# Performance work log

Measured on AMD Instinct MI355X. Metric: run time of the kernel, lower is better.

Reference implementation:

```python
import jax, jax.numpy as jnp
import numpy as np

HEADS = 8
DIM_HEAD = 64
DIM = 512
HIDDEN = HEADS * DIM_HEAD  # 512


def setup_inputs() -> dict:
    key = jax.random.key(0)
    k1, k2, k3, k4 = jax.random.split(key, 4)
    b, m, n = 4, 8, 512
    x = jax.random.normal(k1, (b, m, n, DIM), dtype=jnp.float32)
    pos_bias = jax.random.normal(k2, (HEADS, n, 16, 16), dtype=jnp.float32)
    # torch nn.Linear(dim, 3*hidden) weight is [3*hidden, dim]; we store the
    # transposed matmul form [dim, 3*hidden] for y = x @ W.
    w_qkv = jax.random.normal(k3, (DIM, 3 * HIDDEN), dtype=jnp.float32) * (DIM ** -0.5)
    w_out = jax.random.normal(k4, (HIDDEN, DIM), dtype=jnp.float32) * (HIDDEN ** -0.5)
    return {"x": x, "pos_bias": pos_bias, "w_qkv": w_qkv, "w_out": w_out}


def reference(x, pos_bias, w_qkv, w_out):
    b, m, n, _ = x.shape
    h, d = HEADS, DIM_HEAD
    scale = d ** -0.5
    qkv = jnp.einsum('bmnc,ce->bmne', x, w_qkv)  # [b,m,n,3*hidden]
    q, k, v = jnp.split(qkv, 3, axis=-1)
    # 'b m n (h d) -> (b m) h n d'
    def to_heads(t):
        return t.reshape(b * m, n, h, d).transpose(0, 2, 1, 3)
    q, k, v = to_heads(q), to_heads(k), to_heads(v)
    q = q * scale
    sim = jnp.einsum('bhid,bhjd->bhij', q, k)  # [(b*m), h, n, n]
    # pos_bias [h, n, p, q] -> mean over last two dims -> [h, n] -> broadcast [1,h,n,1]
    pb = pos_bias.mean(axis=(-2, -1))[None, :, :, None]
    sim = sim + pb
    sim = sim - jax.lax.stop_gradient(jnp.max(sim, axis=-1, keepdims=True))
    attn = jax.nn.softmax(sim, axis=-1)
    out = jnp.einsum('bhij,bhjd->bhid', attn, v)  # [(b*m), h, n, d]
    # '(b m) h n d -> b m n (h d)'
    out = out.transpose(0, 2, 1, 3).reshape(b, m, n, h * d)
    return jnp.einsum('bmne,ec->bmnc', out, w_out)
```

## Files before the change

### kernel.cpp

```cpp
#include <hip/hip_runtime.h>
#include <stdint.h>


typedef __attribute__((ext_vector_type(8))) short bf16x8;
typedef __attribute__((ext_vector_type(4))) float f32x4;
typedef __attribute__((ext_vector_type(4))) unsigned short us4;
typedef __attribute__((ext_vector_type(4))) float float4v;

__device__ __forceinline__ unsigned short f2b(float f) {
  union { float f; uint32_t u; } x; x.f = f;
  uint32_t r = x.u + 0x7fffu + ((x.u >> 16) & 1u);
  return (unsigned short)(r >> 16);
}

__device__ __forceinline__ uint32_t cvtpk(float lo, float hi) {
  uint32_t r;
  asm("v_cvt_pk_bf16_f32 %0, %1, %2" : "=v"(r) : "v"(lo), "v"(hi));
  return r;
}

__device__ __forceinline__ f32x4 mfma16(bf16x8 a, bf16x8 b, f32x4 c) {
  return __builtin_amdgcn_mfma_f32_16x16x32_bf16(a, b, c, 0, 0, 0);
}

__device__ __forceinline__ void gload_lds16(const unsigned short* g, unsigned short* l) {
  __builtin_amdgcn_global_load_lds(
      (const __attribute__((address_space(1))) unsigned int*)g,
      (__attribute__((address_space(3))) unsigned int*)l, 16, 0, 0);
}

__global__ __launch_bounds__(256) void cast_x_kernel(
    const float* __restrict__ src, unsigned short* __restrict__ dst) {
  size_t i = ((size_t)blockIdx.x * 256 + threadIdx.x) * 4;
  float4v v = *(const float4v*)(src + i);
  us4 o;
#pragma unroll
  for (int j = 0; j < 4; ++j) o[j] = f2b(v[j]);
  *(us4*)(dst + i) = o;
}

__global__ __launch_bounds__(256) void transpose_cast_kernel(
    const float* __restrict__ src, unsigned short* __restrict__ dst, int R, int C) {
  __shared__ float tile[64][65];
  const int tc0 = blockIdx.x * 64;
  const int tr0 = blockIdx.y * 64;
#pragma unroll
  for (int k2 = 0; k2 < 16; ++k2) {
    int idx = threadIdx.x + k2 * 256;
    int r = idx >> 6, c = idx & 63;
    tile[r][c] = src[(size_t)(tr0 + r) * C + tc0 + c];
  }
  __syncthreads();
#pragma unroll
  for (int k2 = 0; k2 < 16; ++k2) {
    int idx = threadIdx.x + k2 * 256;
    int c = idx >> 6, r = idx & 63;
    dst[(size_t)(tc0 + c) * R + tr0 + r] = f2b(tile[r][c]);
  }
}

__device__ __forceinline__ void gemm_core(
    const unsigned short* __restrict__ A, const unsigned short* __restrict__ Bt,
    int K, int r0, int c0, unsigned short* As, unsigned short* Bs,
    f32x4 (&acc)[4][4]) {
  const int tid = threadIdx.x;
  const int lane = tid & 63;
  const int wave = tid >> 6;
  const int wr = (wave >> 1) * 64;
  const int wc = (wave & 1) * 64;
  const int l15 = lane & 15;
  const int g = lane >> 4;
  const int lsw = l15 & 7;

#pragma unroll
  for (int m = 0; m < 4; ++m)
#pragma unroll
    for (int n = 0; n < 4; ++n) acc[m][n] = (f32x4){0.f, 0.f, 0.f, 0.f};

  for (int kt = 0; kt < K; kt += 64) {
#pragma unroll
    for (int i = 0; i < 4; ++i) {
      int chunk = tid + i * 256;
      int row = chunk >> 3;
      int csw = (chunk & 7) ^ (row & 7);
      gload_lds16(A + (size_t)(r0 + row) * K + kt + csw * 8, As + chunk * 8);
      gload_lds16(Bt + (size_t)(c0 + row) * K + kt + csw * 8, Bs + chunk * 8);
    }
    __syncthreads();
#pragma unroll
    for (int ks = 0; ks < 2; ++ks) {
      bf16x8 af[4], bfr[4];
      const int j = g + ks * 4;
      const int cj = (j ^ lsw) * 8;
#pragma unroll
      for (int m = 0; m < 4; ++m)
        af[m] = *(const bf16x8*)(As + (wr + m * 16 + l15) * 64 + cj);
#pragma unroll
      for (int n = 0; n < 4; ++n)
        bfr[n] = *(const bf16x8*)(Bs + (wc + n * 16 + l15) * 64 + cj);
#pragma unroll
      for (int m = 0; m < 4; ++m)
#pragma unroll
        for (int n = 0; n < 4; ++n) acc[m][n] = mfma16(af[m], bfr[n], acc[m][n]);
    }
    __syncthreads();
  }
}

__global__ __launch_bounds__(256) void gemm_qkv_kernel(
    const unsigned short* __restrict__ xb, const unsigned short* __restrict__ wqbT,
    unsigned short* __restrict__ qb, unsigned short* __restrict__ kb,
    unsigned short* __restrict__ vtb) {
  __shared__ unsigned short smem[16384];
  f32x4 acc[4][4];
  const int r0 = blockIdx.x * 128;
  const int c0 = blockIdx.y * 128;
  gemm_core(xb, wqbT, 512, r0, c0, smem, smem + 8192, acc);

  const int tid = threadIdx.x, lane = tid & 63, wave = tid >> 6;
  const int wr = (wave >> 1) * 64, wc = (wave & 1) * 64;
  const int l15 = lane & 15, g = lane >> 4;
  const int part = c0 >> 9;
  const float scl = (part == 0) ? 0.125f : 1.0f;

  if (part < 2) {
#pragma unroll
    for (int m = 0; m < 4; ++m) {
      int rbase = wr + m * 16 + 4 * g;
#pragma unroll
      for (int n = 0; n < 4; ++n) {
        int c = wc + n * 16 + l15;
        int c2 = c >> 3, ci = c & 7;
#pragma unroll
        for (int rr = 0; rr < 4; ++rr) {
          int r = rbase + rr;
          smem[r * 128 + ((c2 ^ (r & 15)) << 3) + ci] = f2b(acc[m][n][rr] * scl);
        }
      }
    }
    __syncthreads();
    unsigned short* dstb = (part == 0) ? qb : kb;
#pragma unroll
    for (int it = 0; it < 8; ++it) {
      int idx = tid + it * 256;
      int r = idx >> 4, c2 = idx & 15;
      bf16x8 v = *(const bf16x8*)(smem + r * 128 + ((c2 ^ (r & 15)) << 3));
      int e = c0 + c2 * 8;
      int rem = e & 511, h = rem >> 6, d = rem & 63;
      int ig = r0 + r;
      int bh = (ig >> 9) * 8 + h, i = ig & 511;
      *(bf16x8*)(dstb + ((size_t)bh * 512 + i) * 64 + d) = v;
    }
  } else {
#pragma unroll
    for (int m = 0; m < 4; ++m) {
      int rbase = wr + m * 16 + 4 * g;
      int r2 = rbase >> 3, rhalf = rbase & 7;
#pragma unroll
      for (int n = 0; n < 4; ++n) {
        int c = wc + n * 16 + l15;
        us4 v;
#pragma unroll
        for (int rr = 0; rr < 4; ++rr) v[rr] = f2b(acc[m][n][rr]);
        *(us4*)(smem + c * 128 + ((r2 ^ (c & 15)) << 3) + rhalf) = v;
      }
    }
    __syncthreads();
#pragma unroll
    for (int it = 0; it < 8; ++it) {
      int idx = tid + it * 256;
      int c = idx >> 4, r8 = idx & 15;
      bf16x8 v = *(const bf16x8*)(smem + c * 128 + ((r8 ^ (c & 15)) << 3));
      int e = c0 + c;
      int rem = e & 511, h = rem >> 6, d = rem & 63;
      int ig0 = r0 + r8 * 8;
      int bh = (ig0 >> 9) * 8 + h, i = ig0 & 511;
      *(bf16x8*)(vtb + ((size_t)bh * 64 + d) * 512 + i) = v;
    }
  }
}

__global__ __launch_bounds__(256) void gemm_out_kernel(
    const unsigned short* __restrict__ ao, const unsigned short* __restrict__ wobT,
    float* __restrict__ out) {
  __shared__ unsigned short smem[16384];
  f32x4 acc[4][4];
  const int r0 = blockIdx.x * 128;
  const int c0 = blockIdx.y * 128;
  gemm_core(ao, wobT, 512, r0, c0, smem, smem + 8192, acc);

  const int tid = threadIdx.x, lane = tid & 63, wave = tid >> 6;
  const int wr = (wave >> 1) * 64, wc = (wave & 1) * 64;
  const int l15 = lane & 15, g = lane >> 4;
#pragma unroll
  for (int m = 0; m < 4; ++m) {
    int i0g = r0 + wr + m * 16 + 4 * g;
#pragma unroll
    for (int n = 0; n < 4; ++n) {
      int e = c0 + wc + n * 16 + l15;
#pragma unroll
      for (int rr = 0; rr < 4; ++rr)
        out[(size_t)(i0g + rr) * 512 + e] = acc[m][n][rr];
    }
  }
}

__global__ __launch_bounds__(512, 4) void attn_kernel(
    const unsigned short* __restrict__ qb, const unsigned short* __restrict__ kb,
    const unsigned short* __restrict__ vtb, unsigned short* __restrict__ ao) {
  __shared__ unsigned short kbuf[2][8192];
  __shared__ unsigned short vbuf[2][8192];
  __shared__ unsigned short Ps[8][16][40];
  const int bh = blockIdx.x;
  const int qt = blockIdx.y;
  const int tid = threadIdx.x, lane = tid & 63, wave = tid >> 6;
  const int l15 = lane & 15, g = lane >> 4;
  const int qrow0 = qt * 128 + wave * 16;

  const unsigned short* Q = qb + ((size_t)bh * 512 + qrow0) * 64;
  const unsigned short* Kp = kb + (size_t)bh * 512 * 64;
  const unsigned short* Vt = vtb + (size_t)bh * 64 * 512;

  bf16x8 qf0 = *(const bf16x8*)(Q + l15 * 64 + g * 8);
  bf16x8 qf1 = *(const bf16x8*)(Q + l15 * 64 + 32 + g * 8);

  const int krow = tid >> 3;
  const int kck = (tid & 7) ^ (krow & 7);
  const int vrow = tid >> 4;
  const int vck = (tid & 15) ^ (vrow & 15);

  auto stage = [&](int t, int b) {
    const unsigned short* ks = Kp + ((size_t)t * 128 + krow) * 64 + kck * 8;
    gload_lds16(ks, kbuf[b] + tid * 8);
    gload_lds16(ks + 64 * 64, kbuf[b] + tid * 8 + 4096);
    const unsigned short* vs = Vt + (size_t)vrow * 512 + t * 128 + vck * 8;
    gload_lds16(vs, vbuf[b] + tid * 8);
    gload_lds16(vs + 32 * 512, vbuf[b] + tid * 8 + 4096);
  };

  f32x4 oacc[4];
#pragma unroll
  for (int m = 0; m < 4; ++m) oacc[m] = (f32x4){0.f, 0.f, 0.f, 0.f};
  float srow[4] = {0.f, 0.f, 0.f, 0.f};

  stage(0, 0);
  asm volatile("s_waitcnt vmcnt(0)" ::: "memory");
  __builtin_amdgcn_s_barrier();

  int cur = 0;
#pragma unroll
  for (int t = 0; t < 4; ++t) {
    if (t < 3) stage(t + 1, cur ^ 1);

    const unsigned short* kb_ = kbuf[cur];
    f32x4 s[8];
    const int c0i = g ^ (l15 & 7);
    __builtin_amdgcn_s_setprio(1);
#pragma unroll
    for (int tt = 0; tt < 8; ++tt) {
      int row = tt * 16 + l15;
      bf16x8 b0 = *(const bf16x8*)(kb_ + (row * 8 + c0i) * 8);
      bf16x8 b1 = *(const bf16x8*)(kb_ + (row * 8 + (c0i ^ 4)) * 8);
      f32x4 c = (f32x4){0.f, 0.f, 0.f, 0.f};
      c = mfma16(qf0, b0, c);
      s[tt] = mfma16(qf1, b1, c);
    }
    __builtin_amdgcn_s_setprio(0);

#pragma unroll
    for (int tt = 0; tt < 8; ++tt)
#pragma unroll
      for (int rr = 0; rr < 4; ++rr) {
        float e = __expf(s[tt][rr]);
        s[tt][rr] = e;
        srow[rr] += e;
      }

    const unsigned short* vb_ = vbuf[cur];
#pragma unroll
    for (int cc = 0; cc < 4; ++cc) {
#pragma unroll
      for (int rr = 0; rr < 4; ++rr) {
        uint32_t pk = cvtpk(s[cc * 2][rr], s[cc * 2 + 1][rr]);
        Ps[wave][4 * g + rr][l15] = (unsigned short)pk;
        Ps[wave][4 * g + rr][16 + l15] = (unsigned short)(pk >> 16);
      }
      asm volatile("s_waitcnt lgkmcnt(0)" ::: "memory");
      bf16x8 pf = *(const bf16x8*)(&Ps[wave][l15][g * 8]);
      __builtin_amdgcn_s_setprio(1);
#pragma unroll
      for (int m = 0; m < 4; ++m) {
        int vr = m * 16 + l15;
        bf16x8 vf = *(const bf16x8*)(vb_ + (vr * 16 + ((cc * 4 + g) ^ l15)) * 8);
        oacc[m] = mfma16(vf, pf, oacc[m]);
      }
      __builtin_amdgcn_s_setprio(0);
    }

    if (t < 3) {
      asm volatile("s_waitcnt vmcnt(0)" ::: "memory");
      __builtin_amdgcn_s_barrier();
      cur ^= 1;
    }
  }

#pragma unroll
  for (int rr = 0; rr < 4; ++rr)
#pragma unroll
    for (int o = 1; o < 16; o <<= 1) srow[rr] += __shfl_xor(srow[rr], o);
  int srcl = (l15 >> 2) * 16;
  float t0 = __shfl(srow[0], srcl), t1 = __shfl(srow[1], srcl);
  float t2 = __shfl(srow[2], srcl), t3 = __shfl(srow[3], srcl);
  int rq = l15 & 3;
  float sq = rq == 0 ? t0 : rq == 1 ? t1 : rq == 2 ? t2 : t3;
  float invq = 1.0f / sq;

  const int hh = bh & 7, bm = bh >> 3;
  unsigned short* aorow = ao + ((size_t)bm * 512 + qrow0 + l15) * 512 + hh * 64;
#pragma unroll
  for (int m = 0; m < 4; ++m) {
    union { us4 u; uint32_t w[2]; } uv;
    uv.w[0] = cvtpk(oacc[m][0] * invq, oacc[m][1] * invq);
    uv.w[1] = cvtpk(oacc[m][2] * invq, oacc[m][3] * invq);
    *(us4*)(aorow + m * 16 + 4 * g) = uv.u;
  }
}

extern "C" void kernel_launch(void* const* d_in, const int* in_sizes, int n_in,
                              void* d_out, int out_size, void* d_ws, size_t ws_size,
                              hipStream_t stream) {
  const float* x = (const float*)d_in[0];
  const float* w_qkv = (const float*)d_in[2];
  const float* w_out = (const float*)d_in[3];
  float* out = (float*)d_out;

  char* ws = (char*)d_ws;
  const size_t SZ_XB = 16384ull * 512 * 2;
  const size_t SZ_WQ = 1536ull * 512 * 2;
  const size_t SZ_WO = 512ull * 512 * 2;
  const size_t SZ_HB = 256ull * 512 * 64 * 2;
  unsigned short* xb = (unsigned short*)(ws);
  unsigned short* wqbT = (unsigned short*)(ws + SZ_XB);
  unsigned short* wobT = (unsigned short*)(ws + SZ_XB + SZ_WQ);
  unsigned short* qb = (unsigned short*)(ws + SZ_XB + SZ_WQ + SZ_WO);
  unsigned short* kb = (unsigned short*)(ws + SZ_XB + SZ_WQ + SZ_WO + SZ_HB);
  unsigned short* vtb = (unsigned short*)(ws + SZ_XB + SZ_WQ + SZ_WO + 2 * SZ_HB);
  unsigned short* ao = (unsigned short*)(ws + SZ_XB + SZ_WQ + SZ_WO + 3 * SZ_HB);

  cast_x_kernel<<<8192, 256, 0, stream>>>(x, xb);
  transpose_cast_kernel<<<dim3(1536 / 64, 512 / 64), 256, 0, stream>>>(w_qkv, wqbT, 512, 1536);
  transpose_cast_kernel<<<dim3(512 / 64, 512 / 64), 256, 0, stream>>>(w_out, wobT, 512, 512);
  gemm_qkv_kernel<<<dim3(128, 12), 256, 0, stream>>>(xb, wqbT, qb, kb, vtb);
  attn_kernel<<<dim3(256, 4), 512, 0, stream>>>(qb, kb, vtb, ao);
  gemm_out_kernel<<<dim3(128, 4), 256, 0, stream>>>(ao, wobT, out);
}
```

Before: 104.0 us.

## Fuse prep kernels, pipeline GEMM K-loop, shrink attention KV tiles

Merges the x cast and both weight transpose-casts into one launch, and folds the q scale into the transposed weight. The GEMM core becomes a 4-stage, 32-wide K pipeline with partial vmcnt waits, so loads overlap MFMAs. The attention kernel now uses 64-key tiles over 8 iterations with half-size LDS buffers and raised launch bounds to fit more blocks per CU. This trades more barriers and iterations for less launch overhead, better latency hiding and higher occupancy.

```diff
diff --git a/kernel.cpp b/kernel.cpp
--- a/kernel.cpp
+++ b/kernel.cpp
@@ -29,21 +29,34 @@
       (__attribute__((address_space(3))) unsigned int*)l, 16, 0, 0);
 }
 
-__global__ __launch_bounds__(256) void cast_x_kernel(
-    const float* __restrict__ src, unsigned short* __restrict__ dst) {
-  size_t i = ((size_t)blockIdx.x * 256 + threadIdx.x) * 4;
-  float4v v = *(const float4v*)(src + i);
-  us4 o;
-#pragma unroll
-  for (int j = 0; j < 4; ++j) o[j] = f2b(v[j]);
-  *(us4*)(dst + i) = o;
-}
-
-__global__ __launch_bounds__(256) void transpose_cast_kernel(
-    const float* __restrict__ src, unsigned short* __restrict__ dst, int R, int C) {
+__global__ __launch_bounds__(256) void prep_kernel(
+    const float* __restrict__ x, unsigned short* __restrict__ xb,
+    const float* __restrict__ wq, unsigned short* __restrict__ wqbT,
+    const float* __restrict__ wo, unsigned short* __restrict__ wobT) {
+  const int bid = blockIdx.x;
+  if (bid < 8192) {
+    size_t i = ((size_t)bid * 256 + threadIdx.x) * 4;
+    float4v v = *(const float4v*)(x + i);
+    us4 o;
+#pragma unroll
+    for (int j = 0; j < 4; ++j) o[j] = f2b(v[j]);
+    *(us4*)(xb + i) = o;
+    return;
+  }
   __shared__ float tile[64][65];
-  const int tc0 = blockIdx.x * 64;
-  const int tr0 = blockIdx.y * 64;
+  const float* src;
+  unsigned short* dst;
+  int R, C, bx, by;
+  float scl = 1.0f;
+  if (bid < 8192 + 192) {
+    int q = bid - 8192;
+    src = wq; dst = wqbT; R = 512; C = 1536; bx = q % 24; by = q / 24;
+    if (bx * 64 < 512) scl = 0.125f;
+  } else {
+    int q = bid - 8384;
+    src = wo; dst = wobT; R = 512; C = 512; bx = q % 8; by = q / 8;
+  }
+  const int tc0 = bx * 64, tr0 = by * 64;
 #pragma unroll
   for (int k2 = 0; k2 < 16; ++k2) {
     int idx = threadIdx.x + k2 * 256;
@@ -55,13 +68,13 @@
   for (int k2 = 0; k2 < 16; ++k2) {
     int idx = threadIdx.x + k2 * 256;
     int c = idx >> 6, r = idx & 63;
-    dst[(size_t)(tc0 + c) * R + tr0 + r] = f2b(tile[r][c]);
+    dst[(size_t)(tc0 + c) * R + tr0 + r] = f2b(tile[r][c] * scl);
   }
 }
 
 __device__ __forceinline__ void gemm_core(
     const unsigned short* __restrict__ A, const unsigned short* __restrict__ Bt,
-    int K, int r0, int c0, unsigned short* As, unsigned short* Bs,
+    int r0, int c0, unsigned short* As, unsigned short* Bs,
     f32x4 (&acc)[4][4]) {
   const int tid = threadIdx.x;
   const int lane = tid & 63;
@@ -70,58 +83,72 @@
   const int wc = (wave & 1) * 64;
   const int l15 = lane & 15;
   const int g = lane >> 4;
-  const int lsw = l15 & 7;
+  const int rsw = (l15 >> 1) & 3;
 
 #pragma unroll
   for (int m = 0; m < 4; ++m)
 #pragma unroll
     for (int n = 0; n < 4; ++n) acc[m][n] = (f32x4){0.f, 0.f, 0.f, 0.f};
 
-  for (int kt = 0; kt < K; kt += 64) {
-#pragma unroll
-    for (int i = 0; i < 4; ++i) {
+  auto stage_half = [&](int t) {
+    const int off = ((t >> 1) & 1) * 8192 + (t & 1) * 4096;
+    const int kt = t * 32;
+#pragma unroll
+    for (int i = 0; i < 2; ++i) {
       int chunk = tid + i * 256;
-      int row = chunk >> 3;
-      int csw = (chunk & 7) ^ (row & 7);
-      gload_lds16(A + (size_t)(r0 + row) * K + kt + csw * 8, As + chunk * 8);
-      gload_lds16(Bt + (size_t)(c0 + row) * K + kt + csw * 8, Bs + chunk * 8);
-    }
-    __syncthreads();
-#pragma unroll
-    for (int ks = 0; ks < 2; ++ks) {
-      bf16x8 af[4], bfr[4];
-      const int j = g + ks * 4;
-      const int cj = (j ^ lsw) * 8;
-#pragma unroll
-      for (int m = 0; m < 4; ++m)
-        af[m] = *(const bf16x8*)(As + (wr + m * 16 + l15) * 64 + cj);
-#pragma unroll
-      for (int n = 0; n < 4; ++n)
-        bfr[n] = *(const bf16x8*)(Bs + (wc + n * 16 + l15) * 64 + cj);
-#pragma unroll
-      for (int m = 0; m < 4; ++m)
-#pragma unroll
-        for (int n = 0; n < 4; ++n) acc[m][n] = mfma16(af[m], bfr[n], acc[m][n]);
-    }
-    __syncthreads();
-  }
+      int row = chunk >> 2;
+      int cg = (chunk & 3) ^ ((row >> 1) & 3);
+      gload_lds16(A + (size_t)(r0 + row) * 512 + kt + cg * 8, As + off + chunk * 8);
+      gload_lds16(Bt + (size_t)(c0 + row) * 512 + kt + cg * 8, Bs + off + chunk * 8);
+    }
+  };
+
+  stage_half(0);
+  stage_half(1);
+  stage_half(2);
+
+#pragma unroll
+  for (int t = 0; t < 16; ++t) {
+    if (t <= 13)      asm volatile("s_waitcnt vmcnt(8)" ::: "memory");
+    else if (t == 14) asm volatile("s_waitcnt vmcnt(4)" ::: "memory");
+    else              asm volatile("s_waitcnt vmcnt(0)" ::: "memory");
+    __builtin_amdgcn_s_barrier();
+    if (t + 3 < 16) stage_half(t + 3);
+    const int off = ((t >> 1) & 1) * 8192 + (t & 1) * 4096;
+    const unsigned short* as = As + off;
+    const unsigned short* bs = Bs + off;
+    bf16x8 af[4], bfr[4];
+#pragma unroll
+    for (int m = 0; m < 4; ++m)
+      af[m] = *(const bf16x8*)(as + ((wr + m * 16 + l15) * 4 + (g ^ rsw)) * 8);
+#pragma unroll
+    for (int n = 0; n < 4; ++n)
+      bfr[n] = *(const bf16x8*)(bs + ((wc + n * 16 + l15) * 4 + (g ^ rsw)) * 8);
+    __builtin_amdgcn_s_setprio(1);
+#pragma unroll
+    for (int m = 0; m < 4; ++m)
+#pragma unroll
+      for (int n = 0; n < 4; ++n) acc[m][n] = mfma16(af[m], bfr[n], acc[m][n]);
+    __builtin_amdgcn_s_setprio(0);
+  }
+  __syncthreads();
 }
 
 __global__ __launch_bounds__(256) void gemm_qkv_kernel(
     const unsigned short* __restrict__ xb, const unsigned short* __restrict__ wqbT,
     unsigned short* __restrict__ qb, unsigned short* __restrict__ kb,
     unsigned short* __restrict__ vtb) {
-  __shared__ unsigned short smem[16384];
+  __shared__ unsigned short As[16384];
+  __shared__ unsigned short Bs[16384];
   f32x4 acc[4][4];
   const int r0 = blockIdx.x * 128;
   const int c0 = blockIdx.y * 128;
-  gemm_core(xb, wqbT, 512, r0, c0, smem, smem + 8192, acc);
+  gemm_core(xb, wqbT, r0, c0, As, Bs, acc);
 
   const int tid = threadIdx.x, lane = tid & 63, wave = tid >> 6;
   const int wr = (wave >> 1) * 64, wc = (wave & 1) * 64;
   const int l15 = lane & 15, g = lane >> 4;
   const int part = c0 >> 9;
-  const float scl = (part == 0) ? 0.125f : 1.0f;
 
   if (part < 2) {
 #pragma unroll
@@ -134,7 +161,7 @@
 #pragma unroll
         for (int rr = 0; rr < 4; ++rr) {
           int r = rbase + rr;
-          smem[r * 128 + ((c2 ^ (r & 15)) << 3) + ci] = f2b(acc[m][n][rr] * scl);
+          As[r * 128 + ((c2 ^ (r & 15)) << 3) + ci] = f2b(acc[m][n][rr]);
         }
       }
     }
@@ -144,7 +171,7 @@
     for (int it = 0; it < 8; ++it) {
       int idx = tid + it * 256;
       int r = idx >> 4, c2 = idx & 15;
-      bf16x8 v = *(const bf16x8*)(smem + r * 128 + ((c2 ^ (r & 15)) << 3));
+      bf16x8 v = *(const bf16x8*)(As + r * 128 + ((c2 ^ (r & 15)) << 3));
       int e = c0 + c2 * 8;
       int rem = e & 511, h = rem >> 6, d = rem & 63;
       int ig = r0 + r;
@@ -162,7 +189,7 @@
         us4 v;
 #pragma unroll
         for (int rr = 0; rr < 4; ++rr) v[rr] = f2b(acc[m][n][rr]);
-        *(us4*)(smem + c * 128 + ((r2 ^ (c & 15)) << 3) + rhalf) = v;
+        *(us4*)(As + c * 128 + ((r2 ^ (c & 15)) << 3) + rhalf) = v;
       }
     }
     __syncthreads();
@@ -170,7 +197,7 @@
     for (int it = 0; it < 8; ++it) {
       int idx = tid + it * 256;
       int c = idx >> 4, r8 = idx & 15;
-      bf16x8 v = *(const bf16x8*)(smem + c * 128 + ((r8 ^ (c & 15)) << 3));
+      bf16x8 v = *(const bf16x8*)(As + c * 128 + ((r8 ^ (c & 15)) << 3));
       int e = c0 + c;
       int rem = e & 511, h = rem >> 6, d = rem & 63;
       int ig0 = r0 + r8 * 8;
@@ -183,11 +210,12 @@
 __global__ __launch_bounds__(256) void gemm_out_kernel(
     const unsigned short* __restrict__ ao, const unsigned short* __restrict__ wobT,
     float* __restrict__ out) {
-  __shared__ unsigned short smem[16384];
+  __shared__ unsigned short As[16384];
+  __shared__ unsigned short Bs[16384];
   f32x4 acc[4][4];
   const int r0 = blockIdx.x * 128;
   const int c0 = blockIdx.y * 128;
-  gemm_core(ao, wobT, 512, r0, c0, smem, smem + 8192, acc);
+  gemm_core(ao, wobT, r0, c0, As, Bs, acc);
 
   const int tid = threadIdx.x, lane = tid & 63, wave = tid >> 6;
   const int wr = (wave >> 1) * 64, wc = (wave & 1) * 64;
@@ -205,11 +233,11 @@
   }
 }
 
-__global__ __launch_bounds__(512, 4) void attn_kernel(
+__global__ __launch_bounds__(512, 6) void attn_kernel(
     const unsigned short* __restrict__ qb, const unsigned short* __restrict__ kb,
     const unsigned short* __restrict__ vtb, unsigned short* __restrict__ ao) {
-  __shared__ unsigned short kbuf[2][8192];
-  __shared__ unsigned short vbuf[2][8192];
+  __shared__ unsigned short kbuf[2][4096];
+  __shared__ unsigned short vbuf[2][4096];
   __shared__ unsigned short Ps[8][16][40];
   const int bh = blockIdx.x;
   const int qt = blockIdx.y;
@@ -224,24 +252,18 @@
   bf16x8 qf0 = *(const bf16x8*)(Q + l15 * 64 + g * 8);
   bf16x8 qf1 = *(const bf16x8*)(Q + l15 * 64 + 32 + g * 8);
 
-  const int krow = tid >> 3;
-  const int kck = (tid & 7) ^ (krow & 7);
-  const int vrow = tid >> 4;
-  const int vck = (tid & 15) ^ (vrow & 15);
+  const int srow = tid >> 3;
+  const int sck = (tid & 7) ^ (srow & 7);
 
   auto stage = [&](int t, int b) {
-    const unsigned short* ks = Kp + ((size_t)t * 128 + krow) * 64 + kck * 8;
-    gload_lds16(ks, kbuf[b] + tid * 8);
-    gload_lds16(ks + 64 * 64, kbuf[b] + tid * 8 + 4096);
-    const unsigned short* vs = Vt + (size_t)vrow * 512 + t * 128 + vck * 8;
-    gload_lds16(vs, vbuf[b] + tid * 8);
-    gload_lds16(vs + 32 * 512, vbuf[b] + tid * 8 + 4096);
+    gload_lds16(Kp + (size_t)(t * 64 + srow) * 64 + sck * 8, kbuf[b] + tid * 8);
+    gload_lds16(Vt + (size_t)srow * 512 + t * 64 + sck * 8, vbuf[b] + tid * 8);
   };
 
   f32x4 oacc[4];
 #pragma unroll
   for (int m = 0; m < 4; ++m) oacc[m] = (f32x4){0.f, 0.f, 0.f, 0.f};
-  float srow[4] = {0.f, 0.f, 0.f, 0.f};
+  float srowsum[4] = {0.f, 0.f, 0.f, 0.f};
 
   stage(0, 0);
   asm volatile("s_waitcnt vmcnt(0)" ::: "memory");
@@ -249,15 +271,15 @@
 
   int cur = 0;
 #pragma unroll
-  for (int t = 0; t < 4; ++t) {
-    if (t < 3) stage(t + 1, cur ^ 1);
+  for (int t = 0; t < 8; ++t) {
+    if (t < 7) stage(t + 1, cur ^ 1);
 
     const unsigned short* kb_ = kbuf[cur];
-    f32x4 s[8];
+    f32x4 s[4];
     const int c0i = g ^ (l15 & 7);
     __builtin_amdgcn_s_setprio(1);
 #pragma unroll
-    for (int tt = 0; tt < 8; ++tt) {
+    for (int tt = 0; tt < 4; ++tt) {
       int row = tt * 16 + l15;
       bf16x8 b0 = *(const bf16x8*)(kb_ + (row * 8 + c0i) * 8);
       bf16x8 b1 = *(const bf16x8*)(kb_ + (row * 8 + (c0i ^ 4)) * 8);
@@ -268,17 +290,17 @@
     __builtin_amdgcn_s_setprio(0);
 
 #pragma unroll
-    for (int tt = 0; tt < 8; ++tt)
+    for (int tt = 0; tt < 4; ++tt)
 #pragma unroll
       for (int rr = 0; rr < 4; ++rr) {
         float e = __expf(s[tt][rr]);
         s[tt][rr] = e;
-        srow[rr] += e;
+        srowsum[rr] += e;
       }
 
     const unsigned short* vb_ = vbuf[cur];
 #pragma unroll
-    for (int cc = 0; cc < 4; ++cc) {
+    for (int cc = 0; cc < 2; ++cc) {
 #pragma unroll
       for (int rr = 0; rr < 4; ++rr) {
         uint32_t pk = cvtpk(s[cc * 2][rr], s[cc * 2 + 1][rr]);
@@ -291,13 +313,13 @@
 #pragma unroll
       for (int m = 0; m < 4; ++m) {
         int vr = m * 16 + l15;
-        bf16x8 vf = *(const bf16x8*)(vb_ + (vr * 16 + ((cc * 4 + g) ^ l15)) * 8);
+        bf16x8 vf = *(const bf16x8*)(vb_ + (vr * 8 + ((cc * 4 + g) ^ (l15 & 7))) * 8);
         oacc[m] = mfma16(vf, pf, oacc[m]);
       }
       __builtin_amdgcn_s_setprio(0);
     }
 
-    if (t < 3) {
+    if (t < 7) {
       asm volatile("s_waitcnt vmcnt(0)" ::: "memory");
       __builtin_amdgcn_s_barrier();
       cur ^= 1;
@@ -307,10 +329,10 @@
 #pragma unroll
   for (int rr = 0; rr < 4; ++rr)
 #pragma unroll
-    for (int o = 1; o < 16; o <<= 1) srow[rr] += __shfl_xor(srow[rr], o);
+    for (int o = 1; o < 16; o <<= 1) srowsum[rr] += __shfl_xor(srowsum[rr], o);
   int srcl = (l15 >> 2) * 16;
-  float t0 = __shfl(srow[0], srcl), t1 = __shfl(srow[1], srcl);
-  float t2 = __shfl(srow[2], srcl), t3 = __shfl(srow[3], srcl);
+  float t0 = __shfl(srowsum[0], srcl), t1 = __shfl(srowsum[1], srcl);
+  float t2 = __shfl(srowsum[2], srcl), t3 = __shfl(srowsum[3], srcl);
   int rq = l15 & 3;
   float sq = rq == 0 ? t0 : rq == 1 ? t1 : rq == 2 ? t2 : t3;
   float invq = 1.0f / sq;
@@ -347,9 +369,7 @@
   unsigned short* vtb = (unsigned short*)(ws + SZ_XB + SZ_WQ + SZ_WO + 2 * SZ_HB);
   unsigned short* ao = (unsigned short*)(ws + SZ_XB + SZ_WQ + SZ_WO + 3 * SZ_HB);
 
-  cast_x_kernel<<<8192, 256, 0, stream>>>(x, xb);
-  transpose_cast_kernel<<<dim3(1536 / 64, 512 / 64), 256, 0, stream>>>(w_qkv, wqbT, 512, 1536);
-  transpose_cast_kernel<<<dim3(512 / 64, 512 / 64), 256, 0, stream>>>(w_out, wobT, 512, 512);
+  prep_kernel<<<8448, 256, 0, stream>>>(x, xb, w_qkv, wqbT, w_out, wobT);
   gemm_qkv_kernel<<<dim3(128, 12), 256, 0, stream>>>(xb, wqbT, qb, kb, vtb);
   attn_kernel<<<dim3(256, 4), 512, 0, stream>>>(qb, kb, vtb, ao);
   gemm_out_kernel<<<dim3(128, 4), 256, 0, stream>>>(ao, wobT, out);
```

Result: faster. 101.9 us (-2.0%).
